# Optimization experiments

Measured on AMD Instinct MI355X. Metric: run time of the kernel, lower is better.

## Reference

```python
import jax, jax.numpy as jnp
import numpy as np

B, T, D, HD = 256, 256, 512, 64  # batch, seq_len(SEQ_LEN), EMBED_DIM, head_dim


def setup_inputs() -> dict:
    key = jax.random.key(0)
    k1, k2, k3, k4 = jax.random.split(key, 4)
    scale = D ** -0.5  # roughly matches nn.Linear init variance
    return {
        "x": jax.random.normal(k1, (B, T, D), dtype=jnp.float32),
        "Wq": jax.random.normal(k2, (HD, D), dtype=jnp.float32) * scale,
        "Wk": jax.random.normal(k3, (HD, D), dtype=jnp.float32) * scale,
        "Wv": jax.random.normal(k4, (HD, D), dtype=jnp.float32) * scale,
    }


def reference(x, Wq, Wk, Wv):
    # q,k,v: [B, T, HD]  (torch Linear: x @ W.T, no bias)
    q = jnp.einsum("btd,hd->bth", x, Wq)
    k = jnp.einsum("btd,hd->bth", x, Wk)
    v = jnp.einsum("btd,hd->bth", x, Wv)
    head_dim = Wq.shape[0]
    # scores: [B, T, T], scaled by head_dim^-0.5
    scores = jnp.einsum("bqh,bkh->bqk", q, k) * (head_dim ** -0.5)
    T_ = x.shape[1]
    causal = jnp.tril(jnp.ones((T_, T_), dtype=bool))  # tril[:T,:T] == 0 -> -inf
    scores = jnp.where(causal, scores, -jnp.inf)
    attn = jax.nn.softmax(scores, axis=-1)
    # dropout is identity in eval mode (reference baseline)
    return jnp.einsum("bqk,bkh->bqh", attn, v)
```

## Files before the change

kernel.cpp:

```cpp
#include <hip/hip_runtime.h>
#include <hip/hip_bf16.h>
#include <stdint.h>

#define NB 256
#define NT 256
#define ND 512
#define NH 64

typedef __bf16 bf16;
typedef __bf16 bf16x4 __attribute__((ext_vector_type(4)));
typedef __bf16 bf16x8 __attribute__((ext_vector_type(8)));
typedef float f32x4 __attribute__((ext_vector_type(4)));

static __device__ __forceinline__ f32x4 mfma16(bf16x8 a, bf16x8 b, f32x4 c) {
    return __builtin_amdgcn_mfma_f32_16x16x32_bf16(a, b, c, 0, 0, 0);
}

static __device__ __forceinline__ bf16x8 cvt8(f32x4 a, f32x4 b) {
    bf16x8 r;
    r[0] = (bf16)a.x; r[1] = (bf16)a.y; r[2] = (bf16)a.z; r[3] = (bf16)a.w;
    r[4] = (bf16)b.x; r[5] = (bf16)b.y; r[6] = (bf16)b.z; r[7] = (bf16)b.w;
    return r;
}

static __device__ __forceinline__ void gload_lds16(const void* g, void* l) {
    __builtin_amdgcn_global_load_lds(
        (const __attribute__((address_space(1))) void*)g,
        (__attribute__((address_space(3))) void*)l, 16, 0, 0);
}

__global__ __launch_bounds__(256) void wconv_kernel(
        const float* __restrict__ Wq, const float* __restrict__ Wk,
        const float* __restrict__ Wv, bf16* __restrict__ wbf) {
    int idx = (blockIdx.x * 256 + threadIdx.x) * 4;
    const float* src;
    if (idx < 64 * ND)       src = Wq + idx;
    else if (idx < 128 * ND) src = Wk + (idx - 64 * ND);
    else                     src = Wv + (idx - 128 * ND);
    f32x4 v = *reinterpret_cast<const f32x4*>(src);
    bf16x4 o;
    o[0] = (bf16)v.x; o[1] = (bf16)v.y; o[2] = (bf16)v.z; o[3] = (bf16)v.w;
    *reinterpret_cast<bf16x4*>(wbf + idx) = o;
}

__global__ __launch_bounds__(256, 3) void qkv_gemm_kernel(
        const float* __restrict__ x, const bf16* __restrict__ wbf,
        bf16* __restrict__ qws, bf16* __restrict__ kws, bf16* __restrict__ vt) {
    __shared__ alignas(16) char lds[49152];
    const int t = threadIdx.x, lane = t & 63, wave = t >> 6;
    const int l15 = lane & 15, g = lane >> 4;
    const long m0 = (long)blockIdx.x * 64;
    const char* xb = (const char*)x;

    f32x4 acc[4][3] = {};
    bf16x8 Wcur[6], Wnxt[6];

    auto stageDMA = [&](int s) {
        char* base = lds + (s % 3) * 16384;
        #pragma unroll
        for (int i = 0; i < 4; ++i) {
            int row = wave * 16 + i * 4 + g;
            const char* src = xb + (m0 + row) * 2048 + (long)s * 256
                            + ((l15 * 16) ^ ((row & 7) << 4));
            gload_lds16(src, base + (wave * 4 + i) * 1024);
        }
    };
    auto loadW = [&](int s, bf16x8* Wr) {
        #pragma unroll
        for (int ci = 0; ci < 3; ++ci) {
            int n = wave * 48 + ci * 16 + l15;
            const bf16* wsrc = wbf + n * ND + s * 64 + g * 8;
            Wr[ci * 2 + 0] = *reinterpret_cast<const bf16x8*>(wsrc);
            Wr[ci * 2 + 1] = *reinterpret_cast<const bf16x8*>(wsrc + 32);
        }
    };

    loadW(0, Wcur);
    stageDMA(0);
    stageDMA(1);
    asm volatile("s_waitcnt vmcnt(4)" ::: "memory");
    __builtin_amdgcn_s_barrier();

    #pragma unroll
    for (int s = 0; s < 8; ++s) {
        if (s < 7) loadW(s + 1, Wnxt);
        if (s < 6) stageDMA(s + 2);
        char* cbuf = lds + (s % 3) * 16384;
        #pragma unroll
        for (int k2 = 0; k2 < 2; ++k2) {
            const int cbyte = (k2 * 32 + g * 8) * 4;
            bf16x8 Af[4];
            #pragma unroll
            for (int ri = 0; ri < 4; ++ri) {
                int row = ri * 16 + l15;
                int sw = (row & 7) << 4;
                f32x4 lo = *reinterpret_cast<const f32x4*>(cbuf + row * 256 + (cbyte ^ sw));
                f32x4 hi = *reinterpret_cast<const f32x4*>(cbuf + row * 256 + ((cbyte + 16) ^ sw));
                Af[ri] = cvt8(lo, hi);
            }
            #pragma unroll
            for (int ci = 0; ci < 3; ++ci) {
                #pragma unroll
                for (int ri = 0; ri < 4; ++ri)
                    acc[ri][ci] = mfma16(Af[ri], Wcur[ci * 2 + k2], acc[ri][ci]);
            }
        }
        if (s < 7) {
            #pragma unroll
            for (int i = 0; i < 6; ++i) Wcur[i] = Wnxt[i];
            asm volatile("s_waitcnt vmcnt(4)" ::: "memory");
            __builtin_amdgcn_s_barrier();
            asm volatile("" ::: "memory");
        }
    }

    const int b = blockIdx.x >> 2;
    const int tb = (blockIdx.x & 3) * 64;
    #pragma unroll
    for (int ci = 0; ci < 3; ++ci) {
        int n = wave * 48 + ci * 16 + l15;
        int sel = n >> 6, hd = n & 63;
        #pragma unroll
        for (int ri = 0; ri < 4; ++ri) {
            #pragma unroll
            for (int r = 0; r < 4; ++r) {
                int trow = tb + ri * 16 + g * 4 + r;
                long grow = m0 + ri * 16 + g * 4 + r;
                float val = acc[ri][ci][r];
                if (sel == 0)      qws[grow * NH + hd] = (bf16)(val * 0.125f);
                else if (sel == 1) kws[grow * NH + hd] = (bf16)val;
                else               vt[((long)b * NH + hd) * NT + trow] = (bf16)val;
            }
        }
    }
}

__global__ __launch_bounds__(256, 4) void attn_kernel(
        const bf16* __restrict__ qws, const bf16* __restrict__ kws,
        const bf16* __restrict__ vt, float* __restrict__ out) {
    __shared__ alignas(16) char lds[36864];
    const int t = threadIdx.x, lane = t & 63, wave = t >> 6;
    const int l15 = lane & 15, g = lane >> 4;
    const int qb = blockIdx.x, b = blockIdx.y;
    const long bbase = (long)b * NT;
    const int KV = (qb + 1) * 64;

    if (t < KV) {
        const bf16* src = kws + (bbase + t) * NH;
        char* dstrow = lds + t * 128;
        int sw = (t & 7) << 4;
        #pragma unroll
        for (int j = 0; j < 8; ++j) {
            bf16x8 v = *reinterpret_cast<const bf16x8*>(src + j * 8);
            *reinterpret_cast<bf16x8*>(dstrow + ((j * 16) ^ sw)) = v;
        }
    }
    __syncthreads();

    const int qt = qb * 4 + wave;
    const int nct = qt + 1, nch = (nct + 1) >> 1;
    char* plds = lds + 32768 + wave * 1024;

    bf16x8 Qf0, Qf1;
    {
        const bf16* qsrc = qws + (bbase + qt * 16 + l15) * NH + g * 8;
        Qf0 = *reinterpret_cast<const bf16x8*>(qsrc);
        Qf1 = *reinterpret_cast<const bf16x8*>(qsrc + 32);
    }
    const int qrow0 = qt * 16 + g * 4;
    float sum[4] = {0.f, 0.f, 0.f, 0.f};
    f32x4 O[4] = {};

    for (int ch = 0; ch < nch; ++ch) {
        const int c0 = ch * 32 + l15, c1 = c0 + 16;
        const bool t1v = (2 * ch + 1) < nct;
        f32x4 S0 = {}, S1 = {};
        {
            const char* k0p = lds + c0 * 128;
            int sw0 = (c0 & 7) << 4;
            S0 = mfma16(Qf0, *reinterpret_cast<const bf16x8*>(k0p + ((g * 16) ^ sw0)), S0);
            S0 = mfma16(Qf1, *reinterpret_cast<const bf16x8*>(k0p + ((64 + g * 16) ^ sw0)), S0);
            if (t1v) {
                const char* k1p = lds + c1 * 128;
                int sw1 = (c1 & 7) << 4;
                S1 = mfma16(Qf0, *reinterpret_cast<const bf16x8*>(k1p + ((g * 16) ^ sw1)), S1);
                S1 = mfma16(Qf1, *reinterpret_cast<const bf16x8*>(k1p + ((64 + g * 16) ^ sw1)), S1);
            }
        }
        #pragma unroll
        for (int r = 0; r < 4; ++r) {
            int rowp = g * 4 + r;
            int key = ((rowp >> 2) & 3) << 4;
            float p0 = (c0 <= qrow0 + r) ? __expf(S0[r]) : 0.0f;
            sum[r] += p0;
            *reinterpret_cast<bf16*>(plds + rowp * 64 + ((2 * l15) ^ key)) = (bf16)p0;
            float p1 = (t1v && c1 <= qrow0 + r) ? __expf(S1[r]) : 0.0f;
            sum[r] += p1;
            *reinterpret_cast<bf16*>(plds + rowp * 64 + ((2 * (l15 + 16)) ^ key)) = (bf16)p1;
        }
        bf16x8 Pf = *reinterpret_cast<const bf16x8*>(
            plds + l15 * 64 + ((g * 16) ^ (((l15 >> 2) & 3) << 4)));
        const int k0 = ch * 32 + g * 8;
        #pragma unroll
        for (int cb2 = 0; cb2 < 4; ++cb2) {
            int hd = cb2 * 16 + l15;
            bf16x8 Vf = *reinterpret_cast<const bf16x8*>(
                vt + ((long)b * NH + hd) * NT + k0);
            O[cb2] = mfma16(Pf, Vf, O[cb2]);
        }
    }

    #pragma unroll
    for (int r = 0; r < 4; ++r) {
        sum[r] += __shfl_xor(sum[r], 1);
        sum[r] += __shfl_xor(sum[r], 2);
        sum[r] += __shfl_xor(sum[r], 4);
        sum[r] += __shfl_xor(sum[r], 8);
        sum[r] = 1.0f / sum[r];
    }
    #pragma unroll
    for (int cb2 = 0; cb2 < 4; ++cb2) {
        int hd = cb2 * 16 + l15;
        #pragma unroll
        for (int r = 0; r < 4; ++r) {
            long orow = bbase + qt * 16 + g * 4 + r;
            out[orow * NH + hd] = O[cb2][r] * sum[r];
        }
    }
}

extern "C" void kernel_launch(void* const* d_in, const int* in_sizes, int n_in,
                              void* d_out, int out_size, void* d_ws, size_t ws_size,
                              hipStream_t stream) {
    const float* x  = (const float*)d_in[0];
    const float* Wq = (const float*)d_in[1];
    const float* Wk = (const float*)d_in[2];
    const float* Wv = (const float*)d_in[3];
    float* out = (float*)d_out;

    char* ws = (char*)d_ws;
    bf16* wbf = (bf16*)ws;
    bf16* qws = (bf16*)(ws + 0x30000);
    bf16* kws = (bf16*)(ws + 0x30000 + 8388608);
    bf16* vt  = (bf16*)(ws + 0x30000 + 2 * 8388608);

    wconv_kernel<<<96, 256, 0, stream>>>(Wq, Wk, Wv, wbf);
    qkv_gemm_kernel<<<1024, 256, 0, stream>>>(x, wbf, qws, kws, vt);
    attn_kernel<<<dim3(4, NB), 256, 0, stream>>>(qws, kws, vt, out);
}
```

Before: 239.6 us.

## Rewrite QKV GEMM to load x directly into registers per wave, dropping LDS staging

The QKV projection GEMM no longer stages x through a triple-buffered LDS pipeline with barriers. Each wave now owns 32 rows and all 192 output columns, reading x straight from global memory into registers and converting it to bf16. The weight fragments come from global memory (L2-cached) on every chunk. This removes LDS traffic and block-level synchronization and halves the grid, at the cost of higher register pressure (24 accumulators), lower occupancy, and no explicit prefetch of the memory-bound x stream.

```diff
diff --git a/kernel.cpp b/kernel.cpp
--- a/kernel.cpp
+++ b/kernel.cpp
@@ -21,12 +21,6 @@
     r[0] = (bf16)a.x; r[1] = (bf16)a.y; r[2] = (bf16)a.z; r[3] = (bf16)a.w;
     r[4] = (bf16)b.x; r[5] = (bf16)b.y; r[6] = (bf16)b.z; r[7] = (bf16)b.w;
     return r;
-}
-
-static __device__ __forceinline__ void gload_lds16(const void* g, void* l) {
-    __builtin_amdgcn_global_load_lds(
-        (const __attribute__((address_space(1))) void*)g,
-        (__attribute__((address_space(3))) void*)l, 16, 0, 0);
 }
 
 __global__ __launch_bounds__(256) void wconv_kernel(
@@ -43,93 +37,49 @@
     *reinterpret_cast<bf16x4*>(wbf + idx) = o;
 }
 
-__global__ __launch_bounds__(256, 3) void qkv_gemm_kernel(
+__global__ __launch_bounds__(256, 2) void qkv_gemm_kernel(
         const float* __restrict__ x, const bf16* __restrict__ wbf,
         bf16* __restrict__ qws, bf16* __restrict__ kws, bf16* __restrict__ vt) {
-    __shared__ alignas(16) char lds[49152];
     const int t = threadIdx.x, lane = t & 63, wave = t >> 6;
     const int l15 = lane & 15, g = lane >> 4;
-    const long m0 = (long)blockIdx.x * 64;
-    const char* xb = (const char*)x;
-
-    f32x4 acc[4][3] = {};
-    bf16x8 Wcur[6], Wnxt[6];
-
-    auto stageDMA = [&](int s) {
-        char* base = lds + (s % 3) * 16384;
-        #pragma unroll
-        for (int i = 0; i < 4; ++i) {
-            int row = wave * 16 + i * 4 + g;
-            const char* src = xb + (m0 + row) * 2048 + (long)s * 256
-                            + ((l15 * 16) ^ ((row & 7) << 4));
-            gload_lds16(src, base + (wave * 4 + i) * 1024);
-        }
-    };
-    auto loadW = [&](int s, bf16x8* Wr) {
-        #pragma unroll
-        for (int ci = 0; ci < 3; ++ci) {
-            int n = wave * 48 + ci * 16 + l15;
-            const bf16* wsrc = wbf + n * ND + s * 64 + g * 8;
-            Wr[ci * 2 + 0] = *reinterpret_cast<const bf16x8*>(wsrc);
-            Wr[ci * 2 + 1] = *reinterpret_cast<const bf16x8*>(wsrc + 32);
-        }
-    };
-
-    loadW(0, Wcur);
-    stageDMA(0);
-    stageDMA(1);
-    asm volatile("s_waitcnt vmcnt(4)" ::: "memory");
-    __builtin_amdgcn_s_barrier();
-
+    const long m0 = ((long)blockIdx.x * 4 + wave) * 32;
+
+    const float* x0 = x + (m0 + l15) * ND;
+    const float* x1 = x + (m0 + 16 + l15) * ND;
+    const bf16* wb = wbf + l15 * ND + g * 8;
+
+    f32x4 acc[2][12] = {};
+
+    #pragma unroll 2
+    for (int ch = 0; ch < 16; ++ch) {
+        const int k0 = ch * 32 + g * 8;
+        bf16x8 A0 = cvt8(*reinterpret_cast<const f32x4*>(x0 + k0),
+                         *reinterpret_cast<const f32x4*>(x0 + k0 + 4));
+        bf16x8 A1 = cvt8(*reinterpret_cast<const f32x4*>(x1 + k0),
+                         *reinterpret_cast<const f32x4*>(x1 + k0 + 4));
+        #pragma unroll
+        for (int ci = 0; ci < 12; ++ci) {
+            bf16x8 Bf = *reinterpret_cast<const bf16x8*>(wb + ci * 16 * ND + ch * 32);
+            acc[0][ci] = mfma16(A0, Bf, acc[0][ci]);
+            acc[1][ci] = mfma16(A1, Bf, acc[1][ci]);
+        }
+    }
+
+    const int b = (int)(m0 >> 8);
+    const int tb = (int)(m0 & 255);
     #pragma unroll
-    for (int s = 0; s < 8; ++s) {
-        if (s < 7) loadW(s + 1, Wnxt);
-        if (s < 6) stageDMA(s + 2);
-        char* cbuf = lds + (s % 3) * 16384;
-        #pragma unroll
-        for (int k2 = 0; k2 < 2; ++k2) {
-            const int cbyte = (k2 * 32 + g * 8) * 4;
-            bf16x8 Af[4];
-            #pragma unroll
-            for (int ri = 0; ri < 4; ++ri) {
-                int row = ri * 16 + l15;
-                int sw = (row & 7) << 4;
-                f32x4 lo = *reinterpret_cast<const f32x4*>(cbuf + row * 256 + (cbyte ^ sw));
-                f32x4 hi = *reinterpret_cast<const f32x4*>(cbuf + row * 256 + ((cbyte + 16) ^ sw));
-                Af[ri] = cvt8(lo, hi);
-            }
-            #pragma unroll
-            for (int ci = 0; ci < 3; ++ci) {
-                #pragma unroll
-                for (int ri = 0; ri < 4; ++ri)
-                    acc[ri][ci] = mfma16(Af[ri], Wcur[ci * 2 + k2], acc[ri][ci]);
-            }
-        }
-        if (s < 7) {
-            #pragma unroll
-            for (int i = 0; i < 6; ++i) Wcur[i] = Wnxt[i];
-            asm volatile("s_waitcnt vmcnt(4)" ::: "memory");
-            __builtin_amdgcn_s_barrier();
-            asm volatile("" ::: "memory");
-        }
-    }
-
-    const int b = blockIdx.x >> 2;
-    const int tb = (blockIdx.x & 3) * 64;
-    #pragma unroll
-    for (int ci = 0; ci < 3; ++ci) {
-        int n = wave * 48 + ci * 16 + l15;
-        int sel = n >> 6, hd = n & 63;
-        #pragma unroll
-        for (int ri = 0; ri < 4; ++ri) {
+    for (int ci = 0; ci < 12; ++ci) {
+        const int sel = ci >> 2;
+        const int hd = (ci & 3) * 16 + l15;
+        #pragma unroll
+        for (int rt = 0; rt < 2; ++rt) {
             #pragma unroll
             for (int r = 0; r < 4; ++r) {
-                int trow = tb + ri * 16 + g * 4 + r;
-                long grow = m0 + ri * 16 + g * 4 + r;
-                float val = acc[ri][ci][r];
-                if (sel == 0)      qws[grow * NH + hd] = (bf16)(val * 0.125f);
-                else if (sel == 1) kws[grow * NH + hd] = (bf16)val;
-                else               vt[((long)b * NH + hd) * NT + trow] = (bf16)val;
+                const int rr = rt * 16 + g * 4 + r;
+                const float val = acc[rt][ci][r];
+                if (sel == 0)      qws[(m0 + rr) * NH + hd] = (bf16)(val * 0.125f);
+                else if (sel == 1) kws[(m0 + rr) * NH + hd] = (bf16)val;
+                else               vt[((long)b * NH + hd) * NT + tb + rr] = (bf16)val;
             }
         }
     }
@@ -245,6 +195,6 @@
     bf16* vt  = (bf16*)(ws + 0x30000 + 2 * 8388608);
 
     wconv_kernel<<<96, 256, 0, stream>>>(Wq, Wk, Wv, wbf);
-    qkv_gemm_kernel<<<1024, 256, 0, stream>>>(x, wbf, qws, kws, vt);
+    qkv_gemm_kernel<<<512, 256, 0, stream>>>(x, wbf, qws, kws, vt);
     attn_kernel<<<dim3(4, NB), 256, 0, stream>>>(qws, kws, vt, out);
 }
```

Result: slower. 260.1 us (+8.5%).
